# Performance work log

Hardware: AMD Instinct MI355X
Metric: run time of the kernel (lower is better)

The kernel has to match this reference:

```python
import jax, jax.numpy as jnp
import numpy as np

NUM_HEADS = 12
DIM_HEAD = 64
HIDDEN = 768


def _get_rel_pos(size, rel_pos):
    # q_size == k_size: relative coords in [0, 2*size-2]
    idx = jnp.arange(size)[:, None] - jnp.arange(size)[None, :] + (size - 1)
    return rel_pos[idx]  # (size, size, dim_head)


def setup_inputs() -> dict:
    key = jax.random.key(0)
    ks = jax.random.split(key, 5)
    B, H, W, C = 4, 32, 32, HIDDEN
    x = jax.random.normal(ks[0], (B, H, W, C), dtype=jnp.float32)
    w_qkv = jax.random.normal(ks[1], (C, 3 * NUM_HEADS * DIM_HEAD), dtype=jnp.float32) * (C ** -0.5)
    w_out = jax.random.normal(ks[2], (NUM_HEADS * DIM_HEAD, C), dtype=jnp.float32) * ((NUM_HEADS * DIM_HEAD) ** -0.5)
    b_out = jnp.zeros((C,), dtype=jnp.float32)
    rel_pos_h = jax.random.normal(ks[3], (2 * H - 1, DIM_HEAD), dtype=jnp.float32) * 0.02
    rel_pos_w = jax.random.normal(ks[4], (2 * W - 1, DIM_HEAD), dtype=jnp.float32) * 0.02
    return {"x": x, "w_qkv": w_qkv, "w_out": w_out, "b_out": b_out,
            "rel_pos_h": rel_pos_h, "rel_pos_w": rel_pos_w}


def reference(x, w_qkv, w_out, b_out, rel_pos_h, rel_pos_w):
    B, H, W, C = x.shape
    N = H * W
    nh, dh = NUM_HEADS, DIM_HEAD
    # qkv projection: (B, N, 3*nh*dh) split as (qkv, head, dim)
    qkv = x.reshape(B, N, C) @ w_qkv
    qkv = qkv.reshape(B, N, 3, nh, dh).transpose(2, 0, 3, 1, 4)  # (3, B, nh, N, dh)
    q, k, v = qkv[0], qkv[1], qkv[2]
    scale = dh ** -0.5
    attn = jnp.einsum('bhnd,bhmd->bhnm', q, k) * scale  # (B, nh, N, N)
    # decomposed relative positional bias (heads folded into batch)
    Rh = _get_rel_pos(H, rel_pos_h)  # (H, H, dh)
    Rw = _get_rel_pos(W, rel_pos_w)  # (W, W, dh)
    r_q = q.reshape(B * nh, H, W, dh)
    rel_h = jnp.einsum('bhwc,hkc->bhwk', r_q, Rh)  # (B*nh, H, W, H)
    rel_w = jnp.einsum('bhwc,wkc->bhwk', r_q, Rw)  # (B*nh, H, W, W)
    attn = (attn.reshape(B * nh, H, W, H, W)
            + rel_h[:, :, :, :, None]
            + rel_w[:, :, :, None, :]).reshape(B, nh, N, N)
    attn = jax.nn.softmax(attn, axis=-1)
    out = jnp.einsum('bhnm,bhmd->bhnd', attn, v)  # (B, nh, N, dh)
    out = out.transpose(0, 2, 1, 3).reshape(B, N, nh * dh)
    return out @ w_out + b_out  # (B, N, hidden)
```

## Files before the change

kernel.cpp:

```cpp
#include <hip/hip_runtime.h>
#include <cstdint>

#define DEV __device__ __forceinline__

typedef __bf16  bf16x8 __attribute__((ext_vector_type(8)));
typedef short   s16x8  __attribute__((ext_vector_type(8)));
typedef float   f32x4  __attribute__((ext_vector_type(4)));

#define QSCALE 0.18033688011112042f
#define MOFF   17.312340490667560f

DEV unsigned short f2bf(float f){
  union { float f; unsigned u; } v; v.f = f;
  unsigned r = v.u + 0x7fffu + ((v.u >> 16) & 1u);
  return (unsigned short)(r >> 16);
}

DEV unsigned pk2(float lo, float hi){
  unsigned a = __builtin_bit_cast(unsigned, lo) + 0x8000u;
  unsigned b = __builtin_bit_cast(unsigned, hi) + 0x8000u;
  return __builtin_amdgcn_perm(b, a, 0x07060302);
}

DEV void gl2lds16(const void* g, void* l){
  __builtin_amdgcn_global_load_lds((__attribute__((address_space(1))) void*)(void*)(g),
                                   (__attribute__((address_space(3))) void*)(l), 16, 0, 0);
}

DEV f32x4 mfma16(bf16x8 a, bf16x8 b, f32x4 c){
  return __builtin_amdgcn_mfma_f32_16x16x32_bf16(a, b, c, 0, 0, 0);
}

__global__ __launch_bounds__(256) void prep_kernel(const float* __restrict__ x,
                                                   short* __restrict__ xb,
                                                   const float* __restrict__ rph,
                                                   const float* __restrict__ rpw,
                                                   short* __restrict__ rphb,
                                                   short* __restrict__ rpwb,
                                                   const float* __restrict__ w_qkv,
                                                   short* __restrict__ wqT,
                                                   const float* __restrict__ w_out,
                                                   short* __restrict__ woT){
  __shared__ float tb[32][33];
  int b = blockIdx.x;
  if (b < 1536){
    int i = b * 256 + threadIdx.x;
    const float4* in4 = (const float4*)x;
    float4 f0 = in4[i*2], f1 = in4[i*2+1];
    s16x8 o;
    o[0]=(short)f2bf(f0.x); o[1]=(short)f2bf(f0.y); o[2]=(short)f2bf(f0.z); o[3]=(short)f2bf(f0.w);
    o[4]=(short)f2bf(f1.x); o[5]=(short)f2bf(f1.y); o[6]=(short)f2bf(f1.z); o[7]=(short)f2bf(f1.w);
    *(s16x8*)(xb + i*8) = o;
  } else if (b == 1536){
    int t = threadIdx.x;
    for (int j = 0; j < 16; j++){
      int idx = t*16 + j;
      if (idx < 4032){
        rphb[idx] = (short)f2bf(rph[idx] * 8.f);
        rpwb[idx] = (short)f2bf(rpw[idx] * 8.f);
      } else if (idx < 4096){
        rpwb[idx] = 0;
      }
    }
  } else {
    const float* in; short* out; int R, C, bx, by;
    if (b < 3265){ int t = b - 1537; in = w_qkv; out = wqT; R = 768; C = 2304; bx = t % 72; by = t / 72; }
    else         { int t = b - 3265; in = w_out; out = woT; R = 768; C = 768;  bx = t % 24; by = t / 24; }
    int tx = threadIdx.x & 31, ty = threadIdx.x >> 5;
    int c0 = bx * 32, r0 = by * 32;
    for (int i = 0; i < 4; i++)
      tb[ty + i*8][tx] = in[(r0 + ty + i*8)*C + c0 + tx];
    __syncthreads();
    for (int i = 0; i < 4; i++)
      out[(c0 + ty + i*8)*R + r0 + tx] = (short)f2bf(tb[tx][ty + i*8]);
  }
}

__global__ __launch_bounds__(256) void qkv_gemm_kernel(const short* __restrict__ xb,
                                                       const short* __restrict__ wqT,
                                                       short* __restrict__ qb,
                                                       short* __restrict__ kb,
                                                       short* __restrict__ vtb){
  __shared__ __align__(16) short As[128*64];
  __shared__ __align__(16) short Bs[96*64];
  const int tid = threadIdx.x, lane = tid & 63, wv = tid >> 6;
  const int quad = lane >> 4, mi = lane & 15;
  const int flat = blockIdx.x + (blockIdx.y << 5);
  const int xcd = flat & 7, s = flat >> 3;
  const int bx = (xcd & 3)*8 + (s & 7);
  const int by = (xcd >> 2)*12 + (s >> 3);
  const int m0 = bx * 128, n0 = by * 96;
  const int wrow = wv >> 1, wcol = wv & 1;
  const int srow = lane >> 3, scs = lane & 7;
  const int sc = scs ^ (srow & 7);
  f32x4 acc[4][3] = {};
  for (int k0 = 0; k0 < 768; k0 += 64){
    __syncthreads();
    for (int i = 0; i < 4; i++){
      int rbase = i*32 + wv*8;
      int row = rbase + srow;
      gl2lds16(xb + (m0+row)*768 + k0 + sc*8, As + rbase*64 + lane*8);
    }
    for (int i = 0; i < 3; i++){
      int rbase = i*32 + wv*8;
      int row = rbase + srow;
      gl2lds16(wqT + (n0+row)*768 + k0 + sc*8, Bs + rbase*64 + lane*8);
    }
    __syncthreads();
    bf16x8 a[2][4], b[2][3];
#pragma unroll
    for (int kk = 0; kk < 2; kk++){
      int ccs = ((quad + kk*4) ^ (mi & 7)) * 8;
      for (int mt = 0; mt < 4; mt++) a[kk][mt] = *(const bf16x8*)(As + (wrow*64 + mt*16 + mi)*64 + ccs);
      for (int nt = 0; nt < 3; nt++) b[kk][nt] = *(const bf16x8*)(Bs + (wcol*48 + nt*16 + mi)*64 + ccs);
    }
#pragma unroll
    for (int kk = 0; kk < 2; kk++)
      for (int mt = 0; mt < 4; mt++)
        for (int nt = 0; nt < 3; nt++)
          acc[mt][nt] = mfma16(a[kk][mt], b[kk][nt], acc[mt][nt]);
  }
  const int which = n0 / 768;
  if (which == 2){
    for (int nt = 0; nt < 3; nt++){
      int j = n0 + wcol*48 + nt*16 + mi;
      int rem = j % 768;
      int head = rem >> 6, d = rem & 63;
      for (int mt = 0; mt < 4; mt++)
        for (int r = 0; r < 4; r++){
          int m = m0 + wrow*64 + mt*16 + quad*4 + r;
          int bh = (m >> 10)*12 + head;
          vtb[((bh*64 + d) << 10) + (m & 1023)] = (short)f2bf(acc[mt][nt][r]);
        }
    }
  } else {
    const float qs = (which == 0) ? QSCALE : 1.0f;
    short* dst = (which == 0) ? qb : kb;
    for (int nt = 0; nt < 3; nt++){
      int j = n0 + wcol*48 + nt*16 + mi;
      int rem = j % 768;
      int head = rem >> 6, d = rem & 63;
      for (int mt = 0; mt < 4; mt++)
        for (int r = 0; r < 4; r++){
          int m = m0 + wrow*64 + mt*16 + quad*4 + r;
          int bh = (m >> 10)*12 + head;
          dst[((bh << 10) + (m & 1023))*64 + d] = (short)f2bf(acc[mt][nt][r] * qs);
        }
    }
  }
}

__global__ __launch_bounds__(256, 3) void flash_kernel(const short* __restrict__ qb,
                                                       const short* __restrict__ kb,
                                                       const short* __restrict__ vtb,
                                                       const short* __restrict__ rphb,
                                                       const short* __restrict__ rpwb,
                                                       short* __restrict__ ao){
  __shared__ __align__(16) char QE[16384];
  __shared__ __align__(16) short Kt0[64*64];
  __shared__ __align__(16) short Vt0[64*64];
  __shared__ __align__(16) short Pt[64*64];
  __shared__ __align__(16) float rHs[32*64];
  short* Qt  = (short*)QE;
  float* Es  = (float*)QE;
  short* Kt1 = (short*)QE;
  short* Vt1 = (short*)(QE + 8192);
  const int tid = threadIdx.x, lane = tid & 63, wv = tid >> 6;
  const int quad = lane >> 4, mi = lane & 15;
  const int flat = blockIdx.x + (blockIdx.y << 4);
  const int nw = (flat & 7)*96 + (flat >> 3);
  const int bh = nw >> 4, n0 = (nw & 15) << 6;
  const int sw0 = (quad ^ (mi & 7)) * 8;
  const int sw1 = ((quad + 4) ^ (mi & 7)) * 8;
  const int qrow = wv*16 + mi;
  const int srow = lane >> 3;

  const short* kg = kb  + bh*1024*64;
  const short* vg = vtb + bh*64*1024;

#define STAGE(Kd, Vd, stp) do{                                             \
    const short* kt_ = kg + (stp)*4096;                                    \
    _Pragma("unroll")                                                      \
    for (int i_ = 0; i_ < 2; i_++){                                        \
      int slab_ = wv*2 + i_, rbase_ = slab_*8;                             \
      int row_ = rbase_ + srow;                                            \
      int c_ = (lane & 7) ^ (row_ & 7);                                    \
      gl2lds16(kt_ + row_*64 + c_*8, (Kd) + rbase_*64 + lane*8);           \
      gl2lds16(vg + row_*1024 + (stp)*64 + c_*8, (Vd) + rbase_*64 + lane*8);\
    }                                                                      \
  }while(0)

  {
    const short* qg = qb + (bh*1024 + n0)*64;
#pragma unroll
    for (int i = 0; i < 2; i++){
      int slab = wv*2 + i, rbase = slab*8;
      int row = rbase + srow;
      int c = (lane & 7) ^ (row & 7);
      gl2lds16(qg + row*64 + c*8, Qt + rbase*64 + lane*8);
    }
    STAGE(Kt0, Vt0, 0);
  }
  __syncthreads();

  bf16x8 qf0 = *(const bf16x8*)(Qt + qrow*64 + sw0);
  bf16x8 qf1 = *(const bf16x8*)(Qt + qrow*64 + sw1);

  {
    int h = (n0 + wv*16) >> 5;
    const short* rp = rphb + (h + 31 - mi)*64;
#pragma unroll
    for (int khb = 0; khb < 2; khb++){
      const short* rk = rp - khb*1024;
      bf16x8 a0 = *(const bf16x8*)(rk + quad*8);
      bf16x8 a1 = *(const bf16x8*)(rk + 32 + quad*8);
      f32x4 c = {};
      c = mfma16(a0, qf0, c);
      c = mfma16(a1, qf1, c);
      for (int r = 0; r < 4; r++)
        rHs[(khb*16 + quad*4 + r)*64 + wv*16 + mi] = c[r] - MOFF;
    }
  }

  __syncthreads();

#pragma unroll
  for (int jt = 0; jt < 4; jt++){
    const short* rr = rpwb + (jt*16 + mi)*64;
    bf16x8 a0 = *(const bf16x8*)(rr + quad*8);
    bf16x8 a1 = *(const bf16x8*)(rr + 32 + quad*8);
    f32x4 c = {};
    c = mfma16(a0, qf0, c);
    c = mfma16(a1, qf1, c);
    for (int r = 0; r < 4; r++)
      Es[(jt*16 + quad*4 + r)*64 + qrow] = c[r];
  }
  float rw[2][4];
  {
    int w31 = (qrow & 31) + 31;
#pragma unroll
    for (int s = 0; s < 2; s++)
      for (int r = 0; r < 4; r++)
        rw[s][r] = Es[(w31 - (s*16 + quad*4 + r))*64 + qrow];
  }

  __syncthreads();

  f32x4 O[4] = {};
  float l_ = 0.f;

#define COMPUTE(Kb_, Vb_, stp) do{                                          \
    f32x4 S_[4];                                                            \
    _Pragma("unroll")                                                       \
    for (int nt = 0; nt < 4; nt++){                                         \
      bf16x8 kf0 = *(const bf16x8*)((Kb_) + (nt*16 + mi)*64 + sw0);         \
      bf16x8 kf1 = *(const bf16x8*)((Kb_) + (nt*16 + mi)*64 + sw1);         \
      f32x4 c_ = {};                                                        \
      c_ = mfma16(kf0, qf0, c_);                                            \
      c_ = mfma16(kf1, qf1, c_);                                            \
      S_[nt] = c_;                                                          \
    }                                                                       \
    float kh0_ = rHs[(2*(stp))*64 + qrow];                                  \
    float kh1_ = rHs[(2*(stp) + 1)*64 + qrow];                              \
    _Pragma("unroll")                                                       \
    for (int nt = 0; nt < 4; nt++){                                         \
      float kh_ = (nt & 2) ? kh1_ : kh0_;                                   \
      for (int r = 0; r < 4; r++){                                          \
        float p_ = __builtin_amdgcn_exp2f(S_[nt][r] + kh_ + rw[nt & 1][r]); \
        S_[nt][r] = p_;                                                     \
        l_ += p_;                                                           \
      }                                                                     \
    }                                                                       \
    _Pragma("unroll")                                                       \
    for (int nt = 0; nt < 4; nt++){                                         \
      unsigned u0_ = pk2(S_[nt][0], S_[nt][1]);                             \
      unsigned u1_ = pk2(S_[nt][2], S_[nt][3]);                             \
      int chunk_ = (2*nt + (quad >> 1)) ^ (mi & 7);                         \
      uint2 uu_; uu_.x = u0_; uu_.y = u1_;                                  \
      *(uint2*)(Pt + qrow*64 + chunk_*8 + (quad & 1)*4) = uu_;              \
    }                                                                       \
    bf16x8 p0_ = *(const bf16x8*)(Pt + qrow*64 + sw0);                      \
    bf16x8 p1_ = *(const bf16x8*)(Pt + qrow*64 + sw1);                      \
    _Pragma("unroll")                                                       \
    for (int t = 0; t < 4; t++){                                            \
      bf16x8 v0_ = *(const bf16x8*)((Vb_) + (t*16 + mi)*64 + sw0);          \
      bf16x8 v1_ = *(const bf16x8*)((Vb_) + (t*16 + mi)*64 + sw1);          \
      O[t] = mfma16(p0_, v0_, O[t]);                                        \
      O[t] = mfma16(p1_, v1_, O[t]);                                        \
    }                                                                       \
  }while(0)

#pragma unroll 1
  for (int s2 = 0; s2 < 8; s2++){
    STAGE(Kt1, Vt1, 2*s2 + 1);
    COMPUTE(Kt0, Vt0, 2*s2);
    __syncthreads();
    if (s2 < 7) STAGE(Kt0, Vt0, 2*s2 + 2);
    COMPUTE(Kt1, Vt1, 2*s2 + 1);
    if (s2 < 7) __syncthreads();
  }
#undef STAGE
#undef COMPUTE

  l_ += __shfl_xor(l_, 16, 64);
  l_ += __shfl_xor(l_, 32, 64);
  float inv[4];
#pragma unroll
  for (int r = 0; r < 4; r++) inv[r] = 1.f / __shfl(l_, quad*4 + r, 64);
  int b_ = bh / 12, head = bh % 12;
#pragma unroll
  for (int t = 0; t < 4; t++)
    for (int r = 0; r < 4; r++){
      int n = n0 + wv*16 + quad*4 + r;
      ao[(b_*1024 + n)*768 + head*64 + t*16 + mi] = (short)f2bf(O[t][r] * inv[r]);
    }
}

__global__ __launch_bounds__(256) void proj_kernel(const short* __restrict__ ao,
                                                   const short* __restrict__ woT,
                                                   const float* __restrict__ bias,
                                                   float* __restrict__ out){
  __shared__ __align__(16) short As[64*64];
  __shared__ __align__(16) short Bs[96*64];
  const int tid = threadIdx.x, lane = tid & 63, wv = tid >> 6;
  const int quad = lane >> 4, mi = lane & 15;
  const int m0 = blockIdx.x * 64, n0 = blockIdx.y * 96;
  const int wrow = wv >> 1, wcol = wv & 1;
  const int srow = lane >> 3, sc = (lane & 7) ^ (srow & 7);
  f32x4 acc[2][3] = {};
  for (int k0 = 0; k0 < 768; k0 += 64){
    __syncthreads();
    for (int i = 0; i < 2; i++){
      int rbase = i*32 + wv*8, row = rbase + srow;
      gl2lds16(ao + (m0+row)*768 + k0 + sc*8, As + rbase*64 + lane*8);
    }
    for (int i = 0; i < 3; i++){
      int rbase = i*32 + wv*8, row = rbase + srow;
      gl2lds16(woT + (n0+row)*768 + k0 + sc*8, Bs + rbase*64 + lane*8);
    }
    __syncthreads();
    bf16x8 a[2][2], b[2][3];
#pragma unroll
    for (int kk = 0; kk < 2; kk++){
      int ccs = ((quad + kk*4) ^ (mi & 7)) * 8;
      for (int mt = 0; mt < 2; mt++) a[kk][mt] = *(const bf16x8*)(As + (wrow*32 + mt*16 + mi)*64 + ccs);
      for (int nt = 0; nt < 3; nt++) b[kk][nt] = *(const bf16x8*)(Bs + (wcol*48 + nt*16 + mi)*64 + ccs);
    }
#pragma unroll
    for (int kk = 0; kk < 2; kk++)
      for (int mt = 0; mt < 2; mt++)
        for (int nt = 0; nt < 3; nt++)
          acc[mt][nt] = mfma16(a[kk][mt], b[kk][nt], acc[mt][nt]);
  }
  for (int nt = 0; nt < 3; nt++){
    int j = n0 + wcol*48 + nt*16 + mi;
    float bj = bias[j];
    for (int mt = 0; mt < 2; mt++)
      for (int r = 0; r < 4; r++){
        int m = m0 + wrow*32 + mt*16 + quad*4 + r;
        out[m*768 + j] = acc[mt][nt][r] + bj;
      }
  }
}

extern "C" void kernel_launch(void* const* d_in, const int* in_sizes, int n_in,
                              void* d_out, int out_size, void* d_ws, size_t ws_size,
                              hipStream_t stream){
  const float* x     = (const float*)d_in[0];
  const float* w_qkv = (const float*)d_in[1];
  const float* w_out = (const float*)d_in[2];
  const float* b_out = (const float*)d_in[3];
  const float* rph   = (const float*)d_in[4];
  const float* rpw   = (const float*)d_in[5];
  float* out = (float*)d_out;
  char* ws = (char*)d_ws;
  short* xb    = (short*)(ws + 0);
  short* wqT   = (short*)(ws + 6291456);
  short* woT   = (short*)(ws + 9830400);
  short* qb    = (short*)(ws + 11010048);
  short* kb    = (short*)(ws + 17301504);
  short* vtb   = (short*)(ws + 29884416);
  short* rphb  = (short*)(ws + 48758784);
  short* rpwb  = (short*)(ws + 48775168);
  short* ao    = xb;

  prep_kernel<<<3841, 256, 0, stream>>>(x, xb, rph, rpw, rphb, rpwb, w_qkv, wqT, w_out, woT);
  qkv_gemm_kernel<<<dim3(32, 24), 256, 0, stream>>>(xb, wqT, qb, kb, vtb);
  flash_kernel<<<dim3(16, 48), 256, 0, stream>>>(qb, kb, vtb, rphb, rpwb, ao);
  proj_kernel<<<dim3(64, 8), 256, 0, stream>>>(ao, woT, b_out, out);
}
```

Baseline: 151.0 us.

## Fuse QKV GEMM, flash attention and projection into one persistent kernel with grid barriers

Merges the three post-prep kernels into a single 768-block kernel that shares one LDS buffer and separates the phases with atomic-counter grid barriers. The barrier counter is reset in the prep kernel. This removes two kernel launches and the gaps between them. In exchange it depends on all 768 blocks being resident at once (3 per CU), and the spin-wait barriers plus the 256 idle blocks in the projection phase add cost. The in-place reuse of xb as ao is still safe because the barrier orders the phases.

```diff
diff --git a/kernel.cpp b/kernel.cpp
--- a/kernel.cpp
+++ b/kernel.cpp
@@ -29,6 +29,18 @@
 
 DEV f32x4 mfma16(bf16x8 a, bf16x8 b, f32x4 c){
   return __builtin_amdgcn_mfma_f32_16x16x32_bf16(a, b, c, 0, 0, 0);
+}
+
+DEV void gridbar(unsigned* bar, unsigned target){
+  __syncthreads();
+  if (threadIdx.x == 0){
+    __threadfence();
+    atomicAdd(bar, 1u);
+    while (__hip_atomic_load(bar, __ATOMIC_RELAXED, __HIP_MEMORY_SCOPE_AGENT) < target)
+      __builtin_amdgcn_s_sleep(16);
+    __threadfence();
+  }
+  __syncthreads();
 }
 
 __global__ __launch_bounds__(256) void prep_kernel(const float* __restrict__ x,
@@ -40,7 +52,8 @@
                                                    const float* __restrict__ w_qkv,
                                                    short* __restrict__ wqT,
                                                    const float* __restrict__ w_out,
-                                                   short* __restrict__ woT){
+                                                   short* __restrict__ woT,
+                                                   unsigned* __restrict__ bar){
   __shared__ float tb[32][33];
   int b = blockIdx.x;
   if (b < 1536){
@@ -52,6 +65,7 @@
     o[4]=(short)f2bf(f1.x); o[5]=(short)f2bf(f1.y); o[6]=(short)f2bf(f1.z); o[7]=(short)f2bf(f1.w);
     *(s16x8*)(xb + i*8) = o;
   } else if (b == 1536){
+    if (threadIdx.x == 0) *bar = 0;
     int t = threadIdx.x;
     for (int j = 0; j < 16; j++){
       int idx = t*16 + j;
@@ -76,107 +90,107 @@
   }
 }
 
-__global__ __launch_bounds__(256) void qkv_gemm_kernel(const short* __restrict__ xb,
-                                                       const short* __restrict__ wqT,
-                                                       short* __restrict__ qb,
-                                                       short* __restrict__ kb,
-                                                       short* __restrict__ vtb){
-  __shared__ __align__(16) short As[128*64];
-  __shared__ __align__(16) short Bs[96*64];
+__global__ __launch_bounds__(256, 3) void fused_kernel(
+    const short* __restrict__ xb, const short* __restrict__ wqT,
+    short* __restrict__ qb, short* __restrict__ kb, short* __restrict__ vtb,
+    const short* __restrict__ rphb, const short* __restrict__ rpwb,
+    const short* __restrict__ woT, const float* __restrict__ bias,
+    float* __restrict__ out, unsigned* __restrict__ bar)
+{
+  __shared__ __align__(16) char smem[49152];
   const int tid = threadIdx.x, lane = tid & 63, wv = tid >> 6;
   const int quad = lane >> 4, mi = lane & 15;
-  const int flat = blockIdx.x + (blockIdx.y << 5);
-  const int xcd = flat & 7, s = flat >> 3;
-  const int bx = (xcd & 3)*8 + (s & 7);
-  const int by = (xcd >> 2)*12 + (s >> 3);
-  const int m0 = bx * 128, n0 = by * 96;
-  const int wrow = wv >> 1, wcol = wv & 1;
-  const int srow = lane >> 3, scs = lane & 7;
-  const int sc = scs ^ (srow & 7);
-  f32x4 acc[4][3] = {};
-  for (int k0 = 0; k0 < 768; k0 += 64){
-    __syncthreads();
-    for (int i = 0; i < 4; i++){
-      int rbase = i*32 + wv*8;
-      int row = rbase + srow;
-      gl2lds16(xb + (m0+row)*768 + k0 + sc*8, As + rbase*64 + lane*8);
-    }
-    for (int i = 0; i < 3; i++){
-      int rbase = i*32 + wv*8;
-      int row = rbase + srow;
-      gl2lds16(wqT + (n0+row)*768 + k0 + sc*8, Bs + rbase*64 + lane*8);
-    }
-    __syncthreads();
-    bf16x8 a[2][4], b[2][3];
-#pragma unroll
-    for (int kk = 0; kk < 2; kk++){
-      int ccs = ((quad + kk*4) ^ (mi & 7)) * 8;
-      for (int mt = 0; mt < 4; mt++) a[kk][mt] = *(const bf16x8*)(As + (wrow*64 + mt*16 + mi)*64 + ccs);
-      for (int nt = 0; nt < 3; nt++) b[kk][nt] = *(const bf16x8*)(Bs + (wcol*48 + nt*16 + mi)*64 + ccs);
-    }
-#pragma unroll
-    for (int kk = 0; kk < 2; kk++)
-      for (int mt = 0; mt < 4; mt++)
-        for (int nt = 0; nt < 3; nt++)
-          acc[mt][nt] = mfma16(a[kk][mt], b[kk][nt], acc[mt][nt]);
+  const int srow = lane >> 3;
+  const int bid = blockIdx.x;
+  short* ao = (short*)xb;
+
+  {
+    short* As = (short*)smem;
+    short* Bs = (short*)(smem + 16384);
+    const int flat = bid;
+    const int xcd = flat & 7, s = flat >> 3;
+    const int bx = (xcd & 3)*8 + (s & 7);
+    const int by = (xcd >> 2)*12 + (s >> 3);
+    const int m0 = bx * 128, n0 = by * 96;
+    const int wrow = wv >> 1, wcol = wv & 1;
+    const int sc = (lane & 7) ^ (srow & 7);
+    f32x4 acc[4][3] = {};
+    for (int k0 = 0; k0 < 768; k0 += 64){
+      __syncthreads();
+      for (int i = 0; i < 4; i++){
+        int rbase = i*32 + wv*8;
+        int row = rbase + srow;
+        gl2lds16(xb + (m0+row)*768 + k0 + sc*8, As + rbase*64 + lane*8);
+      }
+      for (int i = 0; i < 3; i++){
+        int rbase = i*32 + wv*8;
+        int row = rbase + srow;
+        gl2lds16(wqT + (n0+row)*768 + k0 + sc*8, Bs + rbase*64 + lane*8);
+      }
+      __syncthreads();
+      bf16x8 a[2][4], b[2][3];
+#pragma unroll
+      for (int kk = 0; kk < 2; kk++){
+        int ccs = ((quad + kk*4) ^ (mi & 7)) * 8;
+        for (int mt = 0; mt < 4; mt++) a[kk][mt] = *(const bf16x8*)(As + (wrow*64 + mt*16 + mi)*64 + ccs);
+        for (int nt = 0; nt < 3; nt++) b[kk][nt] = *(const bf16x8*)(Bs + (wcol*48 + nt*16 + mi)*64 + ccs);
+      }
+#pragma unroll
+      for (int kk = 0; kk < 2; kk++)
+        for (int mt = 0; mt < 4; mt++)
+          for (int nt = 0; nt < 3; nt++)
+            acc[mt][nt] = mfma16(a[kk][mt], b[kk][nt], acc[mt][nt]);
+    }
+    const int which = n0 / 768;
+    if (which == 2){
+      for (int nt = 0; nt < 3; nt++){
+        int j = n0 + wcol*48 + nt*16 + mi;
+        int rem = j % 768;
+        int head = rem >> 6, d = rem & 63;
+        for (int mt = 0; mt < 4; mt++)
+          for (int r = 0; r < 4; r++){
+            int m = m0 + wrow*64 + mt*16 + quad*4 + r;
+            int bh = (m >> 10)*12 + head;
+            vtb[((bh*64 + d) << 10) + (m & 1023)] = (short)f2bf(acc[mt][nt][r]);
+          }
+      }
+    } else {
+      const float qs = (which == 0) ? QSCALE : 1.0f;
+      short* dst = (which == 0) ? qb : kb;
+      for (int nt = 0; nt < 3; nt++){
+        int j = n0 + wcol*48 + nt*16 + mi;
+        int rem = j % 768;
+        int head = rem >> 6, d = rem & 63;
+        for (int mt = 0; mt < 4; mt++)
+          for (int r = 0; r < 4; r++){
+            int m = m0 + wrow*64 + mt*16 + quad*4 + r;
+            int bh = (m >> 10)*12 + head;
+            dst[((bh << 10) + (m & 1023))*64 + d] = (short)f2bf(acc[mt][nt][r] * qs);
+          }
+      }
+    }
   }
-  const int which = n0 / 768;
-  if (which == 2){
-    for (int nt = 0; nt < 3; nt++){
-      int j = n0 + wcol*48 + nt*16 + mi;
-      int rem = j % 768;
-      int head = rem >> 6, d = rem & 63;
-      for (int mt = 0; mt < 4; mt++)
-        for (int r = 0; r < 4; r++){
-          int m = m0 + wrow*64 + mt*16 + quad*4 + r;
-          int bh = (m >> 10)*12 + head;
-          vtb[((bh*64 + d) << 10) + (m & 1023)] = (short)f2bf(acc[mt][nt][r]);
-        }
-    }
-  } else {
-    const float qs = (which == 0) ? QSCALE : 1.0f;
-    short* dst = (which == 0) ? qb : kb;
-    for (int nt = 0; nt < 3; nt++){
-      int j = n0 + wcol*48 + nt*16 + mi;
-      int rem = j % 768;
-      int head = rem >> 6, d = rem & 63;
-      for (int mt = 0; mt < 4; mt++)
-        for (int r = 0; r < 4; r++){
-          int m = m0 + wrow*64 + mt*16 + quad*4 + r;
-          int bh = (m >> 10)*12 + head;
-          dst[((bh << 10) + (m & 1023))*64 + d] = (short)f2bf(acc[mt][nt][r] * qs);
-        }
-    }
-  }
-}
-
-__global__ __launch_bounds__(256, 3) void flash_kernel(const short* __restrict__ qb,
-                                                       const short* __restrict__ kb,
-                                                       const short* __restrict__ vtb,
-                                                       const short* __restrict__ rphb,
-                                                       const short* __restrict__ rpwb,
-                                                       short* __restrict__ ao){
-  __shared__ __align__(16) char QE[16384];
-  __shared__ __align__(16) short Kt0[64*64];
-  __shared__ __align__(16) short Vt0[64*64];
-  __shared__ __align__(16) short Pt[64*64];
-  __shared__ __align__(16) float rHs[32*64];
-  short* Qt  = (short*)QE;
-  float* Es  = (float*)QE;
-  short* Kt1 = (short*)QE;
-  short* Vt1 = (short*)(QE + 8192);
-  const int tid = threadIdx.x, lane = tid & 63, wv = tid >> 6;
-  const int quad = lane >> 4, mi = lane & 15;
-  const int flat = blockIdx.x + (blockIdx.y << 4);
-  const int nw = (flat & 7)*96 + (flat >> 3);
-  const int bh = nw >> 4, n0 = (nw & 15) << 6;
-  const int sw0 = (quad ^ (mi & 7)) * 8;
-  const int sw1 = ((quad + 4) ^ (mi & 7)) * 8;
-  const int qrow = wv*16 + mi;
-  const int srow = lane >> 3;
-
-  const short* kg = kb  + bh*1024*64;
-  const short* vg = vtb + bh*64*1024;
+  gridbar(bar, 768);
+
+  {
+    char* QE   = smem;
+    short* Qt  = (short*)QE;
+    float* Es  = (float*)QE;
+    short* Kt1 = (short*)QE;
+    short* Vt1 = (short*)(QE + 8192);
+    short* Kt0 = (short*)(smem + 16384);
+    short* Vt0 = (short*)(smem + 24576);
+    short* Pt  = (short*)(smem + 32768);
+    float* rHs = (float*)(smem + 40960);
+    const int flat = bid;
+    const int nw = (flat & 7)*96 + (flat >> 3);
+    const int bh = nw >> 4, n0 = (nw & 15) << 6;
+    const int sw0 = (quad ^ (mi & 7)) * 8;
+    const int sw1 = ((quad + 4) ^ (mi & 7)) * 8;
+    const int qrow = wv*16 + mi;
+
+    const short* kg = kb  + bh*1024*64;
+    const short* vg = vtb + bh*64*1024;
 
 #define STAGE(Kd, Vd, stp) do{                                             \
     const short* kt_ = kg + (stp)*4096;                                    \
@@ -190,64 +204,64 @@
     }                                                                      \
   }while(0)
 
-  {
-    const short* qg = qb + (bh*1024 + n0)*64;
-#pragma unroll
-    for (int i = 0; i < 2; i++){
-      int slab = wv*2 + i, rbase = slab*8;
-      int row = rbase + srow;
-      int c = (lane & 7) ^ (row & 7);
-      gl2lds16(qg + row*64 + c*8, Qt + rbase*64 + lane*8);
-    }
-    STAGE(Kt0, Vt0, 0);
-  }
-  __syncthreads();
-
-  bf16x8 qf0 = *(const bf16x8*)(Qt + qrow*64 + sw0);
-  bf16x8 qf1 = *(const bf16x8*)(Qt + qrow*64 + sw1);
-
-  {
-    int h = (n0 + wv*16) >> 5;
-    const short* rp = rphb + (h + 31 - mi)*64;
-#pragma unroll
-    for (int khb = 0; khb < 2; khb++){
-      const short* rk = rp - khb*1024;
-      bf16x8 a0 = *(const bf16x8*)(rk + quad*8);
-      bf16x8 a1 = *(const bf16x8*)(rk + 32 + quad*8);
+    {
+      const short* qg = qb + (bh*1024 + n0)*64;
+#pragma unroll
+      for (int i = 0; i < 2; i++){
+        int slab = wv*2 + i, rbase = slab*8;
+        int row = rbase + srow;
+        int c = (lane & 7) ^ (row & 7);
+        gl2lds16(qg + row*64 + c*8, Qt + rbase*64 + lane*8);
+      }
+      STAGE(Kt0, Vt0, 0);
+    }
+    __syncthreads();
+
+    bf16x8 qf0 = *(const bf16x8*)(Qt + qrow*64 + sw0);
+    bf16x8 qf1 = *(const bf16x8*)(Qt + qrow*64 + sw1);
+
+    {
+      int h = (n0 + wv*16) >> 5;
+      const short* rp = rphb + (h + 31 - mi)*64;
+#pragma unroll
+      for (int khb = 0; khb < 2; khb++){
+        const short* rk = rp - khb*1024;
+        bf16x8 a0 = *(const bf16x8*)(rk + quad*8);
+        bf16x8 a1 = *(const bf16x8*)(rk + 32 + quad*8);
+        f32x4 c = {};
+        c = mfma16(a0, qf0, c);
+        c = mfma16(a1, qf1, c);
+        for (int r = 0; r < 4; r++)
+          rHs[(khb*16 + quad*4 + r)*64 + wv*16 + mi] = c[r] - MOFF;
+      }
+    }
+
+    __syncthreads();
+
+#pragma unroll
+    for (int jt = 0; jt < 4; jt++){
+      const short* rr = rpwb + (jt*16 + mi)*64;
+      bf16x8 a0 = *(const bf16x8*)(rr + quad*8);
+      bf16x8 a1 = *(const bf16x8*)(rr + 32 + quad*8);
       f32x4 c = {};
       c = mfma16(a0, qf0, c);
       c = mfma16(a1, qf1, c);
       for (int r = 0; r < 4; r++)
-        rHs[(khb*16 + quad*4 + r)*64 + wv*16 + mi] = c[r] - MOFF;
-    }
-  }
-
-  __syncthreads();
-
-#pragma unroll
-  for (int jt = 0; jt < 4; jt++){
-    const short* rr = rpwb + (jt*16 + mi)*64;
-    bf16x8 a0 = *(const bf16x8*)(rr + quad*8);
-    bf16x8 a1 = *(const bf16x8*)(rr + 32 + quad*8);
-    f32x4 c = {};
-    c = mfma16(a0, qf0, c);
-    c = mfma16(a1, qf1, c);
-    for (int r = 0; r < 4; r++)
-      Es[(jt*16 + quad*4 + r)*64 + qrow] = c[r];
-  }
-  float rw[2][4];
-  {
-    int w31 = (qrow & 31) + 31;
-#pragma unroll
-    for (int s = 0; s < 2; s++)
-      for (int r = 0; r < 4; r++)
-        rw[s][r] = Es[(w31 - (s*16 + quad*4 + r))*64 + qrow];
-  }
-
-  __syncthreads();
-
-  f32x4 O[4] = {};
-  float l_ = 0.f;
+        Es[(jt*16 + quad*4 + r)*64 + qrow] = c[r];
+    }
+    float rw[2][4];
+    {
+      int w31 = (qrow & 31) + 31;
+#pragma unroll
+      for (int s = 0; s < 2; s++)
+        for (int r = 0; r < 4; r++)
+          rw[s][r] = Es[(w31 - (s*16 + quad*4 + r))*64 + qrow];
+    }
+
+    __syncthreads();
+
+    f32x4 O[4] = {};
+    float l_ = 0.f;
 
 #define COMPUTE(Kb_, Vb_, stp) do{                                          \
     f32x4 S_[4];                                                            \
@@ -291,75 +305,72 @@
   }while(0)
 
 #pragma unroll 1
-  for (int s2 = 0; s2 < 8; s2++){
-    STAGE(Kt1, Vt1, 2*s2 + 1);
-    COMPUTE(Kt0, Vt0, 2*s2);
-    __syncthreads();
-    if (s2 < 7) STAGE(Kt0, Vt0, 2*s2 + 2);
-    COMPUTE(Kt1, Vt1, 2*s2 + 1);
-    if (s2 < 7) __syncthreads();
-  }
+    for (int s2 = 0; s2 < 8; s2++){
+      STAGE(Kt1, Vt1, 2*s2 + 1);
+      COMPUTE(Kt0, Vt0, 2*s2);
+      __syncthreads();
+      if (s2 < 7) STAGE(Kt0, Vt0, 2*s2 + 2);
+      COMPUTE(Kt1, Vt1, 2*s2 + 1);
+      if (s2 < 7) __syncthreads();
+    }
 #undef STAGE
 #undef COMPUTE
 
-  l_ += __shfl_xor(l_, 16, 64);
-  l_ += __shfl_xor(l_, 32, 64);
-  float inv[4];
-#pragma unroll
-  for (int r = 0; r < 4; r++) inv[r] = 1.f / __shfl(l_, quad*4 + r, 64);
-  int b_ = bh / 12, head = bh % 12;
-#pragma unroll
-  for (int t = 0; t < 4; t++)
-    for (int r = 0; r < 4; r++){
-      int n = n0 + wv*16 + quad*4 + r;
-      ao[(b_*1024 + n)*768 + head*64 + t*16 + mi] = (short)f2bf(O[t][r] * inv[r]);
-    }
-}
-
-__global__ __launch_bounds__(256) void proj_kernel(const short* __restrict__ ao,
-                                                   const short* __restrict__ woT,
-                                                   const float* __restrict__ bias,
-                                                   float* __restrict__ out){
-  __shared__ __align__(16) short As[64*64];
-  __shared__ __align__(16) short Bs[96*64];
-  const int tid = threadIdx.x, lane = tid & 63, wv = tid >> 6;
-  const int quad = lane >> 4, mi = lane & 15;
-  const int m0 = blockIdx.x * 64, n0 = blockIdx.y * 96;
-  const int wrow = wv >> 1, wcol = wv & 1;
-  const int srow = lane >> 3, sc = (lane & 7) ^ (srow & 7);
-  f32x4 acc[2][3] = {};
-  for (int k0 = 0; k0 < 768; k0 += 64){
-    __syncthreads();
-    for (int i = 0; i < 2; i++){
-      int rbase = i*32 + wv*8, row = rbase + srow;
-      gl2lds16(ao + (m0+row)*768 + k0 + sc*8, As + rbase*64 + lane*8);
-    }
-    for (int i = 0; i < 3; i++){
-      int rbase = i*32 + wv*8, row = rbase + srow;
-      gl2lds16(woT + (n0+row)*768 + k0 + sc*8, Bs + rbase*64 + lane*8);
-    }
-    __syncthreads();
-    bf16x8 a[2][2], b[2][3];
-#pragma unroll
-    for (int kk = 0; kk < 2; kk++){
-      int ccs = ((quad + kk*4) ^ (mi & 7)) * 8;
-      for (int mt = 0; mt < 2; mt++) a[kk][mt] = *(const bf16x8*)(As + (wrow*32 + mt*16 + mi)*64 + ccs);
-      for (int nt = 0; nt < 3; nt++) b[kk][nt] = *(const bf16x8*)(Bs + (wcol*48 + nt*16 + mi)*64 + ccs);
-    }
-#pragma unroll
-    for (int kk = 0; kk < 2; kk++)
+    l_ += __shfl_xor(l_, 16, 64);
+    l_ += __shfl_xor(l_, 32, 64);
+    float inv[4];
+#pragma unroll
+    for (int r = 0; r < 4; r++) inv[r] = 1.f / __shfl(l_, quad*4 + r, 64);
+    int b_ = bh / 12, head = bh % 12;
+#pragma unroll
+    for (int t = 0; t < 4; t++)
+      for (int r = 0; r < 4; r++){
+        int n = n0 + wv*16 + quad*4 + r;
+        ao[(b_*1024 + n)*768 + head*64 + t*16 + mi] = (short)f2bf(O[t][r] * inv[r]);
+      }
+  }
+  gridbar(bar, 1536);
+
+  if (bid < 512){
+    short* As = (short*)smem;
+    short* Bs = (short*)(smem + 8192);
+    const int m0 = (bid & 63) * 64, n0 = (bid >> 6) * 96;
+    const int wrow = wv >> 1, wcol = wv & 1;
+    const int sc = (lane & 7) ^ (srow & 7);
+    f32x4 acc[2][3] = {};
+    for (int k0 = 0; k0 < 768; k0 += 64){
+      __syncthreads();
+      for (int i = 0; i < 2; i++){
+        int rbase = i*32 + wv*8, row = rbase + srow;
+        gl2lds16(ao + (m0+row)*768 + k0 + sc*8, As + rbase*64 + lane*8);
+      }
+      for (int i = 0; i < 3; i++){
+        int rbase = i*32 + wv*8, row = rbase + srow;
+        gl2lds16(woT + (n0+row)*768 + k0 + sc*8, Bs + rbase*64 + lane*8);
+      }
+      __syncthreads();
+      bf16x8 a[2][2], b[2][3];
+#pragma unroll
+      for (int kk = 0; kk < 2; kk++){
+        int ccs = ((quad + kk*4) ^ (mi & 7)) * 8;
+        for (int mt = 0; mt < 2; mt++) a[kk][mt] = *(const bf16x8*)(As + (wrow*32 + mt*16 + mi)*64 + ccs);
+        for (int nt = 0; nt < 3; nt++) b[kk][nt] = *(const bf16x8*)(Bs + (wcol*48 + nt*16 + mi)*64 + ccs);
+      }
+#pragma unroll
+      for (int kk = 0; kk < 2; kk++)
+        for (int mt = 0; mt < 2; mt++)
+          for (int nt = 0; nt < 3; nt++)
+            acc[mt][nt] = mfma16(a[kk][mt], b[kk][nt], acc[mt][nt]);
+    }
+    for (int nt = 0; nt < 3; nt++){
+      int j = n0 + wcol*48 + nt*16 + mi;
+      float bj = bias[j];
       for (int mt = 0; mt < 2; mt++)
-        for (int nt = 0; nt < 3; nt++)
-          acc[mt][nt] = mfma16(a[kk][mt], b[kk][nt], acc[mt][nt]);
-  }
-  for (int nt = 0; nt < 3; nt++){
-    int j = n0 + wcol*48 + nt*16 + mi;
-    float bj = bias[j];
-    for (int mt = 0; mt < 2; mt++)
-      for (int r = 0; r < 4; r++){
-        int m = m0 + wrow*32 + mt*16 + quad*4 + r;
-        out[m*768 + j] = acc[mt][nt][r] + bj;
-      }
+        for (int r = 0; r < 4; r++){
+          int m = m0 + wrow*32 + mt*16 + quad*4 + r;
+          out[m*768 + j] = acc[mt][nt][r] + bj;
+        }
+    }
   }
 }
 
@@ -382,10 +393,10 @@
   short* vtb   = (short*)(ws + 29884416);
   short* rphb  = (short*)(ws + 48758784);
   short* rpwb  = (short*)(ws + 48775168);
-  short* ao    = xb;
-
-  prep_kernel<<<3841, 256, 0, stream>>>(x, xb, rph, rpw, rphb, rpwb, w_qkv, wqT, w_out, woT);
-  qkv_gemm_kernel<<<dim3(32, 24), 256, 0, stream>>>(xb, wqT, qb, kb, vtb);
-  flash_kernel<<<dim3(16, 48), 256, 0, stream>>>(qb, kb, vtb, rphb, rpwb, ao);
-  proj_kernel<<<dim3(64, 8), 256, 0, stream>>>(ao, woT, b_out, out);
-}
+  unsigned* bar = (unsigned*)(ws + 48791552);
+
+  prep_kernel<<<3841, 256, 0, stream>>>(x, xb, rph, rpw, rphb, rpwb,
+                                        w_qkv, wqT, w_out, woT, bar);
+  fused_kernel<<<768, 256, 0, stream>>>(xb, wqT, qb, kb, vtb, rphb, rpwb,
+                                        woT, b_out, out, bar);
+}
```

New measurement: 328.5 us. 2.17x slower.

## Process two query row tiles per wave in flash kernel with 128-thread blocks

Applied to the files above, without the earlier changes.

The flash attention kernel now uses 2 waves per block, and each wave handles 32 query rows as two 16-row tiles. Each K and V fragment read from LDS is reused for both tiles, halving LDS reads of K/V per MFMA. The cost is roughly double the registers per wave for accumulators and S tiles, fewer waves per block to hide latency, and a changed launch bound of (128,2) that may limit occupancy.

```diff
diff --git a/kernel.cpp b/kernel.cpp
--- a/kernel.cpp
+++ b/kernel.cpp
@@ -91,8 +91,8 @@
   const int by = (xcd >> 2)*12 + (s >> 3);
   const int m0 = bx * 128, n0 = by * 96;
   const int wrow = wv >> 1, wcol = wv & 1;
-  const int srow = lane >> 3, scs = lane & 7;
-  const int sc = scs ^ (srow & 7);
+  const int srow = lane >> 3;
+  const int sc = (lane & 7) ^ (srow & 7);
   f32x4 acc[4][3] = {};
   for (int k0 = 0; k0 < 768; k0 += 64){
     __syncthreads();
@@ -150,7 +150,7 @@
   }
 }
 
-__global__ __launch_bounds__(256, 3) void flash_kernel(const short* __restrict__ qb,
+__global__ __launch_bounds__(128, 2) void flash_kernel(const short* __restrict__ qb,
                                                        const short* __restrict__ kb,
                                                        const short* __restrict__ vtb,
                                                        const short* __restrict__ rphb,
@@ -167,34 +167,35 @@
   short* Vt1 = (short*)(QE + 8192);
   const int tid = threadIdx.x, lane = tid & 63, wv = tid >> 6;
   const int quad = lane >> 4, mi = lane & 15;
+  const int srow = lane >> 3;
   const int flat = blockIdx.x + (blockIdx.y << 4);
   const int nw = (flat & 7)*96 + (flat >> 3);
   const int bh = nw >> 4, n0 = (nw & 15) << 6;
   const int sw0 = (quad ^ (mi & 7)) * 8;
   const int sw1 = ((quad + 4) ^ (mi & 7)) * 8;
-  const int qrow = wv*16 + mi;
-  const int srow = lane >> 3;
+  const int q0 = wv*32 + mi;
+  const int q1 = wv*32 + 16 + mi;
 
   const short* kg = kb  + bh*1024*64;
   const short* vg = vtb + bh*64*1024;
 
-#define STAGE(Kd, Vd, stp) do{                                             \
-    const short* kt_ = kg + (stp)*4096;                                    \
-    _Pragma("unroll")                                                      \
-    for (int i_ = 0; i_ < 2; i_++){                                        \
-      int slab_ = wv*2 + i_, rbase_ = slab_*8;                             \
-      int row_ = rbase_ + srow;                                            \
-      int c_ = (lane & 7) ^ (row_ & 7);                                    \
-      gl2lds16(kt_ + row_*64 + c_*8, (Kd) + rbase_*64 + lane*8);           \
+#define STAGE(Kd, Vd, stp) do{                                              \
+    const short* kt_ = kg + (stp)*4096;                                     \
+    _Pragma("unroll")                                                       \
+    for (int i_ = 0; i_ < 4; i_++){                                         \
+      int slab_ = wv*4 + i_, rbase_ = slab_*8;                              \
+      int row_ = rbase_ + srow;                                             \
+      int c_ = (lane & 7) ^ (row_ & 7);                                     \
+      gl2lds16(kt_ + row_*64 + c_*8, (Kd) + rbase_*64 + lane*8);            \
       gl2lds16(vg + row_*1024 + (stp)*64 + c_*8, (Vd) + rbase_*64 + lane*8);\
-    }                                                                      \
+    }                                                                       \
   }while(0)
 
   {
     const short* qg = qb + (bh*1024 + n0)*64;
 #pragma unroll
-    for (int i = 0; i < 2; i++){
-      int slab = wv*2 + i, rbase = slab*8;
+    for (int i = 0; i < 4; i++){
+      int slab = wv*4 + i, rbase = slab*8;
       int row = rbase + srow;
       int c = (lane & 7) ^ (row & 7);
       gl2lds16(qg + row*64 + c*8, Qt + rbase*64 + lane*8);
@@ -203,22 +204,26 @@
   }
   __syncthreads();
 
-  bf16x8 qf0 = *(const bf16x8*)(Qt + qrow*64 + sw0);
-  bf16x8 qf1 = *(const bf16x8*)(Qt + qrow*64 + sw1);
+  bf16x8 qA0 = *(const bf16x8*)(Qt + q0*64 + sw0);
+  bf16x8 qA1 = *(const bf16x8*)(Qt + q0*64 + sw1);
+  bf16x8 qB0 = *(const bf16x8*)(Qt + q1*64 + sw0);
+  bf16x8 qB1 = *(const bf16x8*)(Qt + q1*64 + sw1);
 
   {
-    int h = (n0 + wv*16) >> 5;
+    int h = (n0 + wv*32) >> 5;
     const short* rp = rphb + (h + 31 - mi)*64;
 #pragma unroll
     for (int khb = 0; khb < 2; khb++){
       const short* rk = rp - khb*1024;
       bf16x8 a0 = *(const bf16x8*)(rk + quad*8);
       bf16x8 a1 = *(const bf16x8*)(rk + 32 + quad*8);
-      f32x4 c = {};
-      c = mfma16(a0, qf0, c);
-      c = mfma16(a1, qf1, c);
-      for (int r = 0; r < 4; r++)
-        rHs[(khb*16 + quad*4 + r)*64 + wv*16 + mi] = c[r] - MOFF;
+      f32x4 cA = {}, cB = {};
+      cA = mfma16(a0, qA0, cA); cA = mfma16(a1, qA1, cA);
+      cB = mfma16(a0, qB0, cB); cB = mfma16(a1, qB1, cB);
+      for (int r = 0; r < 4; r++){
+        rHs[(khb*16 + quad*4 + r)*64 + wv*32 + mi]      = cA[r] - MOFF;
+        rHs[(khb*16 + quad*4 + r)*64 + wv*32 + 16 + mi] = cB[r] - MOFF;
+      }
     }
   }
 
@@ -229,64 +234,74 @@
     const short* rr = rpwb + (jt*16 + mi)*64;
     bf16x8 a0 = *(const bf16x8*)(rr + quad*8);
     bf16x8 a1 = *(const bf16x8*)(rr + 32 + quad*8);
-    f32x4 c = {};
-    c = mfma16(a0, qf0, c);
-    c = mfma16(a1, qf1, c);
-    for (int r = 0; r < 4; r++)
-      Es[(jt*16 + quad*4 + r)*64 + qrow] = c[r];
-  }
-  float rw[2][4];
+    f32x4 cA = {}, cB = {};
+    cA = mfma16(a0, qA0, cA); cA = mfma16(a1, qA1, cA);
+    cB = mfma16(a0, qB0, cB); cB = mfma16(a1, qB1, cB);
+    for (int r = 0; r < 4; r++){
+      Es[(jt*16 + quad*4 + r)*64 + q0] = cA[r];
+      Es[(jt*16 + quad*4 + r)*64 + q1] = cB[r];
+    }
+  }
+  float rwA[2][4], rwB[2][4];
   {
-    int w31 = (qrow & 31) + 31;
+    int wA = (q0 & 31) + 31, wB = (q1 & 31) + 31;
 #pragma unroll
     for (int s = 0; s < 2; s++)
-      for (int r = 0; r < 4; r++)
-        rw[s][r] = Es[(w31 - (s*16 + quad*4 + r))*64 + qrow];
+      for (int r = 0; r < 4; r++){
+        rwA[s][r] = Es[(wA - (s*16 + quad*4 + r))*64 + q0];
+        rwB[s][r] = Es[(wB - (s*16 + quad*4 + r))*64 + q1];
+      }
   }
 
   __syncthreads();
 
-  f32x4 O[4] = {};
-  float l_ = 0.f;
+  f32x4 OA[4] = {}, OB[4] = {};
+  float lA = 0.f, lB = 0.f;
 
 #define COMPUTE(Kb_, Vb_, stp) do{                                          \
-    f32x4 S_[4];                                                            \
+    f32x4 SA[4], SB[4];                                                     \
     _Pragma("unroll")                                                       \
     for (int nt = 0; nt < 4; nt++){                                         \
       bf16x8 kf0 = *(const bf16x8*)((Kb_) + (nt*16 + mi)*64 + sw0);         \
       bf16x8 kf1 = *(const bf16x8*)((Kb_) + (nt*16 + mi)*64 + sw1);         \
-      f32x4 c_ = {};                                                        \
-      c_ = mfma16(kf0, qf0, c_);                                            \
-      c_ = mfma16(kf1, qf1, c_);                                            \
-      S_[nt] = c_;                                                          \
+      f32x4 cA = {}; cA = mfma16(kf0, qA0, cA); cA = mfma16(kf1, qA1, cA);  \
+      SA[nt] = cA;                                                          \
+      f32x4 cB = {}; cB = mfma16(kf0, qB0, cB); cB = mfma16(kf1, qB1, cB);  \
+      SB[nt] = cB;                                                          \
     }                                                                       \
-    float kh0_ = rHs[(2*(stp))*64 + qrow];                                  \
-    float kh1_ = rHs[(2*(stp) + 1)*64 + qrow];                              \
+    float khA0 = rHs[(2*(stp))*64 + q0], khA1 = rHs[(2*(stp)+1)*64 + q0];   \
+    float khB0 = rHs[(2*(stp))*64 + q1], khB1 = rHs[(2*(stp)+1)*64 + q1];   \
     _Pragma("unroll")                                                       \
     for (int nt = 0; nt < 4; nt++){                                         \
-      float kh_ = (nt & 2) ? kh1_ : kh0_;                                   \
+      float khA = (nt & 2) ? khA1 : khA0;                                   \
+      float khB = (nt & 2) ? khB1 : khB0;                                   \
       for (int r = 0; r < 4; r++){                                          \
-        float p_ = __builtin_amdgcn_exp2f(S_[nt][r] + kh_ + rw[nt & 1][r]); \
-        S_[nt][r] = p_;                                                     \
-        l_ += p_;                                                           \
+        float pA = __builtin_amdgcn_exp2f(SA[nt][r] + khA + rwA[nt&1][r]);  \
+        SA[nt][r] = pA; lA += pA;                                           \
+        float pB = __builtin_amdgcn_exp2f(SB[nt][r] + khB + rwB[nt&1][r]);  \
+        SB[nt][r] = pB; lB += pB;                                           \
       }                                                                     \
     }                                                                       \
     _Pragma("unroll")                                                       \
     for (int nt = 0; nt < 4; nt++){                                         \
-      unsigned u0_ = pk2(S_[nt][0], S_[nt][1]);                             \
-      unsigned u1_ = pk2(S_[nt][2], S_[nt][3]);                             \
       int chunk_ = (2*nt + (quad >> 1)) ^ (mi & 7);                         \
-      uint2 uu_; uu_.x = u0_; uu_.y = u1_;                                  \
-      *(uint2*)(Pt + qrow*64 + chunk_*8 + (quad & 1)*4) = uu_;              \
+      uint2 uA; uA.x = pk2(SA[nt][0], SA[nt][1]);                           \
+      uA.y = pk2(SA[nt][2], SA[nt][3]);                                     \
+      *(uint2*)(Pt + q0*64 + chunk_*8 + (quad & 1)*4) = uA;                 \
+      uint2 uB; uB.x = pk2(SB[nt][0], SB[nt][1]);                           \
+      uB.y = pk2(SB[nt][2], SB[nt][3]);                                     \
+      *(uint2*)(Pt + q1*64 + chunk_*8 + (quad & 1)*4) = uB;                 \
     }                                                                       \
-    bf16x8 p0_ = *(const bf16x8*)(Pt + qrow*64 + sw0);                      \
-    bf16x8 p1_ = *(const bf16x8*)(Pt + qrow*64 + sw1);                      \
+    bf16x8 pA0 = *(const bf16x8*)(Pt + q0*64 + sw0);                        \
+    bf16x8 pA1 = *(const bf16x8*)(Pt + q0*64 + sw1);                        \
+    bf16x8 pB0 = *(const bf16x8*)(Pt + q1*64 + sw0);                        \
+    bf16x8 pB1 = *(const bf16x8*)(Pt + q1*64 + sw1);                        \
     _Pragma("unroll")                                                       \
     for (int t = 0; t < 4; t++){                                            \
-      bf16x8 v0_ = *(const bf16x8*)((Vb_) + (t*16 + mi)*64 + sw0);          \
-      bf16x8 v1_ = *(const bf16x8*)((Vb_) + (t*16 + mi)*64 + sw1);          \
-      O[t] = mfma16(p0_, v0_, O[t]);                                        \
-      O[t] = mfma16(p1_, v1_, O[t]);                                        \
+      bf16x8 v0 = *(const bf16x8*)((Vb_) + (t*16 + mi)*64 + sw0);           \
+      bf16x8 v1 = *(const bf16x8*)((Vb_) + (t*16 + mi)*64 + sw1);           \
+      OA[t] = mfma16(pA0, v0, OA[t]); OA[t] = mfma16(pA1, v1, OA[t]);       \
+      OB[t] = mfma16(pB0, v0, OB[t]); OB[t] = mfma16(pB1, v1, OB[t]);       \
     }                                                                       \
   }while(0)
 
@@ -302,17 +317,22 @@
 #undef STAGE
 #undef COMPUTE
 
-  l_ += __shfl_xor(l_, 16, 64);
-  l_ += __shfl_xor(l_, 32, 64);
-  float inv[4];
-#pragma unroll
-  for (int r = 0; r < 4; r++) inv[r] = 1.f / __shfl(l_, quad*4 + r, 64);
+  lA += __shfl_xor(lA, 16, 64); lA += __shfl_xor(lA, 32, 64);
+  lB += __shfl_xor(lB, 16, 64); lB += __shfl_xor(lB, 32, 64);
+  float invA[4], invB[4];
+#pragma unroll
+  for (int r = 0; r < 4; r++){
+    invA[r] = 1.f / __shfl(lA, quad*4 + r, 64);
+    invB[r] = 1.f / __shfl(lB, quad*4 + r, 64);
+  }
   int b_ = bh / 12, head = bh % 12;
 #pragma unroll
   for (int t = 0; t < 4; t++)
     for (int r = 0; r < 4; r++){
-      int n = n0 + wv*16 + quad*4 + r;
-      ao[(b_*1024 + n)*768 + head*64 + t*16 + mi] = (short)f2bf(O[t][r] * inv[r]);
+      int nA = n0 + wv*32 + quad*4 + r;
+      int nB = nA + 16;
+      ao[(b_*1024 + nA)*768 + head*64 + t*16 + mi] = (short)f2bf(OA[t][r] * invA[r]);
+      ao[(b_*1024 + nB)*768 + head*64 + t*16 + mi] = (short)f2bf(OB[t][r] * invB[r]);
     }
 }
 
@@ -386,6 +406,6 @@
 
   prep_kernel<<<3841, 256, 0, stream>>>(x, xb, rph, rpw, rphb, rpwb, w_qkv, wqT, w_out, woT);
   qkv_gemm_kernel<<<dim3(32, 24), 256, 0, stream>>>(xb, wqT, qb, kb, vtb);
-  flash_kernel<<<dim3(16, 48), 256, 0, stream>>>(qb, kb, vtb, rphb, rpwb, ao);
+  flash_kernel<<<dim3(16, 48), 128, 0, stream>>>(qb, kb, vtb, rphb, rpwb, ao);
   proj_kernel<<<dim3(64, 8), 256, 0, stream>>>(ao, woT, b_out, out);
 }
```

Measured after the change: 153.1 us. About the same (+1.4%).

## Triple-buffer K/V tiles in flash kernel with vmcnt-gated barriers

Applied to the files above, without the earlier changes.

Replaces the double-buffered K/V staging with a three-stage ring buffer in 64KB of LDS. The loop is fully unrolled and the global-to-LDS copies are waited on with partial vmcnt waits plus raw s_barrier, so two tiles stay in flight while one is computed. The goal is to hide global load latency better. In exchange, LDS use per block rises and launch bounds drop from 3 to 2 blocks per CU, which lowers occupancy. Correctness depends on the Q/Es/rHs LDS aliasing and on the vmcnt counts matching the number of outstanding loads.

```diff
diff --git a/kernel.cpp b/kernel.cpp
--- a/kernel.cpp
+++ b/kernel.cpp
@@ -91,8 +91,8 @@
   const int by = (xcd >> 2)*12 + (s >> 3);
   const int m0 = bx * 128, n0 = by * 96;
   const int wrow = wv >> 1, wcol = wv & 1;
-  const int srow = lane >> 3, scs = lane & 7;
-  const int sc = scs ^ (srow & 7);
+  const int srow = lane >> 3;
+  const int sc = (lane & 7) ^ (srow & 7);
   f32x4 acc[4][3] = {};
   for (int k0 = 0; k0 < 768; k0 += 64){
     __syncthreads();
@@ -150,21 +150,23 @@
   }
 }
 
-__global__ __launch_bounds__(256, 3) void flash_kernel(const short* __restrict__ qb,
+__global__ __launch_bounds__(256, 2) void flash_kernel(const short* __restrict__ qb,
                                                        const short* __restrict__ kb,
                                                        const short* __restrict__ vtb,
                                                        const short* __restrict__ rphb,
                                                        const short* __restrict__ rpwb,
                                                        short* __restrict__ ao){
-  __shared__ __align__(16) char QE[16384];
-  __shared__ __align__(16) short Kt0[64*64];
-  __shared__ __align__(16) short Vt0[64*64];
-  __shared__ __align__(16) short Pt[64*64];
-  __shared__ __align__(16) float rHs[32*64];
-  short* Qt  = (short*)QE;
-  float* Es  = (float*)QE;
-  short* Kt1 = (short*)QE;
-  short* Vt1 = (short*)(QE + 8192);
+  __shared__ __align__(16) char smem[65536];
+  short* K0 = (short*)smem;
+  short* V0 = (short*)(smem + 8192);
+  short* K1 = (short*)(smem + 16384);
+  short* V1 = (short*)(smem + 24576);
+  short* K2 = (short*)(smem + 32768);
+  short* V2 = (short*)(smem + 40960);
+  short* Pt = (short*)(smem + 49152);
+  float* rHs= (float*)(smem + 57344);
+  short* Qt = (short*)smem;
+  float* Es = (float*)smem;
   const int tid = threadIdx.x, lane = tid & 63, wv = tid >> 6;
   const int quad = lane >> 4, mi = lane & 15;
   const int flat = blockIdx.x + (blockIdx.y << 4);
@@ -199,7 +201,6 @@
       int c = (lane & 7) ^ (row & 7);
       gl2lds16(qg + row*64 + c*8, Qt + rbase*64 + lane*8);
     }
-    STAGE(Kt0, Vt0, 0);
   }
   __syncthreads();
 
@@ -290,17 +291,35 @@
     }                                                                       \
   }while(0)
 
-#pragma unroll 1
-  for (int s2 = 0; s2 < 8; s2++){
-    STAGE(Kt1, Vt1, 2*s2 + 1);
-    COMPUTE(Kt0, Vt0, 2*s2);
-    __syncthreads();
-    if (s2 < 7) STAGE(Kt0, Vt0, 2*s2 + 2);
-    COMPUTE(Kt1, Vt1, 2*s2 + 1);
-    if (s2 < 7) __syncthreads();
-  }
+#define SYNC8() asm volatile("s_waitcnt vmcnt(8)\n\ts_barrier" ::: "memory")
+#define SYNC4() asm volatile("s_waitcnt vmcnt(4)\n\ts_barrier" ::: "memory")
+#define SYNC0() asm volatile("s_waitcnt vmcnt(0)\n\ts_barrier" ::: "memory")
+#define DBAR()  asm volatile("s_barrier" ::: "memory")
+
+  STAGE(K0, V0, 0);
+  STAGE(K1, V1, 1);
+  STAGE(K2, V2, 2);  SYNC8(); COMPUTE(K0, V0, 0);  DBAR();
+  STAGE(K0, V0, 3);  SYNC8(); COMPUTE(K1, V1, 1);  DBAR();
+  STAGE(K1, V1, 4);  SYNC8(); COMPUTE(K2, V2, 2);  DBAR();
+  STAGE(K2, V2, 5);  SYNC8(); COMPUTE(K0, V0, 3);  DBAR();
+  STAGE(K0, V0, 6);  SYNC8(); COMPUTE(K1, V1, 4);  DBAR();
+  STAGE(K1, V1, 7);  SYNC8(); COMPUTE(K2, V2, 5);  DBAR();
+  STAGE(K2, V2, 8);  SYNC8(); COMPUTE(K0, V0, 6);  DBAR();
+  STAGE(K0, V0, 9);  SYNC8(); COMPUTE(K1, V1, 7);  DBAR();
+  STAGE(K1, V1, 10); SYNC8(); COMPUTE(K2, V2, 8);  DBAR();
+  STAGE(K2, V2, 11); SYNC8(); COMPUTE(K0, V0, 9);  DBAR();
+  STAGE(K0, V0, 12); SYNC8(); COMPUTE(K1, V1, 10); DBAR();
+  STAGE(K1, V1, 13); SYNC8(); COMPUTE(K2, V2, 11); DBAR();
+  STAGE(K2, V2, 14); SYNC8(); COMPUTE(K0, V0, 12); DBAR();
+  STAGE(K0, V0, 15); SYNC8(); COMPUTE(K1, V1, 13);
+                     SYNC4(); COMPUTE(K2, V2, 14);
+                     SYNC0(); COMPUTE(K0, V0, 15);
 #undef STAGE
 #undef COMPUTE
+#undef SYNC8
+#undef SYNC4
+#undef SYNC0
+#undef DBAR
 
   l_ += __shfl_xor(l_, 16, 64);
   l_ += __shfl_xor(l_, 32, 64);
```

Measured after the change: 151.5 us. No clear change (+0.3%).
